# Performance work log

Measured on AMD Instinct MI355X. Metric: run time of the kernel, lower is better.

Reference implementation:

```python
import jax, jax.numpy as jnp
import numpy as np

N_NODES = 50000
N_EDGES = 600000
IN_DIM = 128
HID = 128
N_LAYERS = 4
N_GRAPHS = 128
N_CLASSES = 10
SPARSITY = 0.5
BN_EPS = 1e-5


def setup_inputs() -> dict:
    key = jax.random.key(0)
    ks = jax.random.split(key, 16)
    h = jax.random.normal(ks[0], (N_NODES, IN_DIM), dtype=jnp.float32)
    snorm_n = jax.random.uniform(ks[1], (N_NODES, 1), dtype=jnp.float32)
    src = jax.random.randint(ks[2], (N_EDGES,), 0, N_NODES, dtype=jnp.int32)
    dst = jax.random.randint(ks[3], (N_EDGES,), 0, N_NODES, dtype=jnp.int32)
    graph_ids = jnp.sort(jax.random.randint(ks[4], (N_NODES,), 0, N_GRAPHS, dtype=jnp.int32))
    # Expander (sparsity-masked) linear params
    embed_W = 0.1 * jax.random.normal(ks[5], (HID, IN_DIM), dtype=jnp.float32)
    embed_mask = (jax.random.uniform(ks[6], (HID, IN_DIM)) < SPARSITY).astype(jnp.float32)
    embed_b = jnp.zeros((HID,), dtype=jnp.float32)
    layer_W = 0.1 * jax.random.normal(ks[7], (N_LAYERS, HID, HID), dtype=jnp.float32)
    layer_mask = (jax.random.uniform(ks[8], (N_LAYERS, HID, HID)) < SPARSITY).astype(jnp.float32)
    layer_b = jnp.zeros((N_LAYERS, HID), dtype=jnp.float32)
    gamma = jnp.ones((N_LAYERS, HID), dtype=jnp.float32)
    beta = jnp.zeros((N_LAYERS, HID), dtype=jnp.float32)
    ro_W = 0.1 * jax.random.normal(ks[9], (N_CLASSES, HID), dtype=jnp.float32)
    ro_b = jnp.zeros((N_CLASSES,), dtype=jnp.float32)
    return {"h": h, "snorm_n": snorm_n, "src": src, "dst": dst, "graph_ids": graph_ids,
            "embed_W": embed_W, "embed_mask": embed_mask, "embed_b": embed_b,
            "layer_W": layer_W, "layer_mask": layer_mask, "layer_b": layer_b,
            "gamma": gamma, "beta": beta, "ro_W": ro_W, "ro_b": ro_b}


def reference(h, snorm_n, src, dst, graph_ids, embed_W, embed_mask, embed_b,
              layer_W, layer_mask, layer_b, gamma, beta, ro_W, ro_b):
    n = h.shape[0]
    # embedding_h: sparsity-masked linear
    h = h @ (embed_W * embed_mask).T + embed_b
    for l in range(layer_W.shape[0]):
        h_in = h
        # message passing: copy_src + sum reduce over edges
        agg = jax.ops.segment_sum(h[src], dst, num_segments=n)  # [N, HID]
        # node apply: masked linear MLP (n_mlp=1)
        z = agg @ (layer_W[l] * layer_mask[l]).T + layer_b[l]
        # graph norm
        z = z * snorm_n
        # batch norm (training-mode batch statistics)
        mu = jnp.mean(z, axis=0)
        var = jnp.var(z, axis=0)
        z = (z - mu) * jax.lax.rsqrt(var + BN_EPS) * gamma[l] + beta[l]
        # activation + residual
        z = jax.nn.relu(z)
        h = h_in + z
    # mean readout over graphs (segment mean)
    sums = jax.ops.segment_sum(h, graph_ids, num_segments=N_GRAPHS)  # [G, HID]
    cnt = jax.ops.segment_sum(jnp.ones((n, 1), h.dtype), graph_ids, num_segments=N_GRAPHS)
    hg = sums / jnp.maximum(cnt, 1.0)
    return hg @ ro_W.T + ro_b
```

## Files before the change

### kernel.cpp

```cpp
#include <hip/hip_runtime.h>
#include <hip/hip_bf16.h>

#define N_NODES   50000
#define N_EDGES   600000
#define HID       128
#define N_LAYERS  4
#define N_GRAPHS  128
#define N_CLASSES 10
#define BN_EPS    1e-5f

#define RSPLIT 8
#define SCAN_B 196
#define GEMM_GRID ((N_NODES + 63) / 64)
#define CVT_N   3200000
#define CVT_GRID ((CVT_N + 255) / 256)
#define NREP 32

#define OFF_WMT   0u
#define OFF_H     81920u
#define OFF_Z     (OFF_H   + 6400000u)
#define OFF_AGG   (OFF_Z   + 6400000u)
#define OFF_ZERO  (OFF_AGG + 6400000u)
#define OFF_CSUMR OFF_ZERO
#define OFF_SUMS  (OFF_CSUMR + 32768u)
#define OFF_DEG   (OFF_SUMS + 16384u)
#define ZERO_N    (32768u + 16384u + 50000u)
#define OFF_OFFS  (OFF_ZERO + ZERO_N)
#define OFF_POS   (OFF_OFFS + 50004u)
#define OFF_ESRC  (OFF_POS  + 50000u)
#define OFF_GST   (OFF_ESRC + 600000u)
#define OFF_BSUM  (OFF_GST  + 132u)
#define OFF_TOT   (OFF_BSUM + 196u)
#define OFF_CSUMF (OFF_TOT  + 4u)
#define OFF_HBF   (OFF_CSUMF + 1024u)

#define PRE_ZB 388
#define PRE_WB 160
#define PRE_BB 196

typedef __attribute__((ext_vector_type(8))) short short8;
typedef __attribute__((ext_vector_type(4))) float f32x4;

__device__ __forceinline__ unsigned int bf16_of(float f) {
    unsigned int u = __float_as_uint(f);
    return (u + 0x7fffu + ((u >> 16) & 1u)) >> 16;
}
__device__ __forceinline__ unsigned int pack_bf2(float lo, float hi) {
    return bf16_of(lo) | (bf16_of(hi) << 16);
}

__global__ __launch_bounds__(256) void preamble_kernel(
    int* __restrict__ zbase,
    const float* __restrict__ We, const float* __restrict__ Me,
    const float* __restrict__ Wl, const float* __restrict__ Ml,
    unsigned int* __restrict__ Wbf,
    const int* __restrict__ gid, int* __restrict__ g_start)
{
    int b = blockIdx.x;
    if (b < PRE_ZB) {
        int i = b * 256 + threadIdx.x;
        if (i < (int)ZERO_N) zbase[i] = 0;
    } else if (b < PRE_ZB + PRE_WB) {
        int i = (b - PRE_ZB) * 256 + threadIdx.x;
        if (i < 5 * 8192) {
            int m = i >> 13;
            int j = i & 8191;
            int c = j >> 6, ku = j & 63;
            const float* Wsrc = (m == 0) ? We : Wl + (m - 1) * 16384;
            const float* Msrc = (m == 0) ? Me : Ml + (m - 1) * 16384;
            int base = c * 128 + ku * 2;
            float w0 = Wsrc[base] * Msrc[base];
            float w1 = Wsrc[base + 1] * Msrc[base + 1];
            unsigned int h0 = bf16_of(w0), h1 = bf16_of(w1);
            float l0 = w0 - __uint_as_float(h0 << 16);
            float l1 = w1 - __uint_as_float(h1 << 16);
            Wbf[m * 16384 + c * 64 + ku]        = h0 | (h1 << 16);
            Wbf[m * 16384 + 8192 + c * 64 + ku] = bf16_of(l0) | (bf16_of(l1) << 16);
        }
    } else {
        int i = (b - PRE_ZB - PRE_WB) * 256 + threadIdx.x;
        if (i >= N_NODES) return;
        int g = gid[i];
        if (i == 0) {
            for (int x = 0; x <= g; ++x) g_start[x] = 0;
        } else {
            int gp = gid[i - 1];
            for (int x = gp + 1; x <= g; ++x) g_start[x] = i;
        }
        if (i == N_NODES - 1) {
            for (int x = g + 1; x <= N_GRAPHS; ++x) g_start[x] = N_NODES;
        }
    }
}

__global__ __launch_bounds__(256) void cvt_kernel(const float2* __restrict__ src,
                                                  unsigned int* __restrict__ dst, int n) {
    int i = blockIdx.x * 256 + threadIdx.x;
    if (i < n) {
        float2 v = src[i];
        dst[i] = pack_bf2(v.x, v.y);
    }
}

__global__ __launch_bounds__(256) void hist_kernel(const int* __restrict__ dst,
                                                   int* __restrict__ deg, int nE) {
    int i = blockIdx.x * 256 + threadIdx.x;
    if (i < nE) atomicAdd(&deg[dst[i]], 1);
}

__global__ __launch_bounds__(256) void scan1_kernel(const int* __restrict__ deg,
                                                    int* __restrict__ off,
                                                    int* __restrict__ bsum, int n) {
    __shared__ int s[256];
    int tid = threadIdx.x;
    int i = blockIdx.x * 256 + tid;
    int v = (i < n) ? deg[i] : 0;
    s[tid] = v;
    __syncthreads();
#pragma unroll
    for (int ofs = 1; ofs < 256; ofs <<= 1) {
        int t = (tid >= ofs) ? s[tid - ofs] : 0;
        __syncthreads();
        s[tid] += t;
        __syncthreads();
    }
    if (i < n) off[i] = s[tid] - v;
    if (tid == 255) bsum[blockIdx.x] = s[255];
}

__global__ __launch_bounds__(256) void scan2_kernel(int* __restrict__ bsum,
                                                    int* __restrict__ total, int nb) {
    __shared__ int s[256];
    int tid = threadIdx.x;
    int v = (tid < nb) ? bsum[tid] : 0;
    s[tid] = v;
    __syncthreads();
#pragma unroll
    for (int ofs = 1; ofs < 256; ofs <<= 1) {
        int t = (tid >= ofs) ? s[tid - ofs] : 0;
        __syncthreads();
        s[tid] += t;
        __syncthreads();
    }
    if (tid < nb) bsum[tid] = s[tid] - v;
    if (tid == 255) *total = s[255];
}

__global__ __launch_bounds__(256) void scan3_kernel(int* __restrict__ off,
                                                    const int* __restrict__ bsum,
                                                    const int* __restrict__ total,
                                                    int* __restrict__ pos, int n) {
    int i = blockIdx.x * 256 + threadIdx.x;
    if (i < n) {
        int o = off[i] + bsum[blockIdx.x];
        off[i] = o;
        pos[i] = o;
    }
    if (i == 0) off[n] = *total;
}

__global__ __launch_bounds__(256) void fill_kernel(const int* __restrict__ src,
                                                   const int* __restrict__ dst,
                                                   int* __restrict__ pos,
                                                   int* __restrict__ esrc, int nE) {
    int i = blockIdx.x * 256 + threadIdx.x;
    if (i < nE) {
        int p = atomicAdd(&pos[dst[i]], 1);
        esrc[p] = src[i];
    }
}

__global__ __launch_bounds__(256) void aggregate_kernel(const unsigned int* __restrict__ Hbf,
                                                        const int* __restrict__ off,
                                                        const int* __restrict__ esrc,
                                                        unsigned int* __restrict__ aggbf,
                                                        int nN) {
    int wid  = (blockIdx.x * 256 + threadIdx.x) >> 6;
    int lane = threadIdx.x & 63;
    int half = lane >> 5;
    int l4   = lane & 31;
    int node = wid * 2 + half;
    if (node >= nN) return;
    int beg = off[node], end = off[node + 1];
    const uint2* H2 = (const uint2*)Hbf;
    float4 a0 = make_float4(0.f, 0.f, 0.f, 0.f);
    float4 a1 = make_float4(0.f, 0.f, 0.f, 0.f);
    float4 a2 = make_float4(0.f, 0.f, 0.f, 0.f);
    float4 a3 = make_float4(0.f, 0.f, 0.f, 0.f);
#define ACCUM(AX, V)                                                        \
    AX.x += __uint_as_float((V).x << 16);                                   \
    AX.y += __uint_as_float((V).x & 0xffff0000u);                           \
    AX.z += __uint_as_float((V).y << 16);                                   \
    AX.w += __uint_as_float((V).y & 0xffff0000u);
    int e = beg;
    for (; e + 7 < end; e += 8) {
        int s0 = esrc[e],     s1 = esrc[e + 1], s2 = esrc[e + 2], s3 = esrc[e + 3];
        int s4 = esrc[e + 4], s5 = esrc[e + 5], s6 = esrc[e + 6], s7 = esrc[e + 7];
        uint2 v0 = H2[(size_t)s0 * 32 + l4];
        uint2 v1 = H2[(size_t)s1 * 32 + l4];
        uint2 v2 = H2[(size_t)s2 * 32 + l4];
        uint2 v3 = H2[(size_t)s3 * 32 + l4];
        uint2 v4 = H2[(size_t)s4 * 32 + l4];
        uint2 v5 = H2[(size_t)s5 * 32 + l4];
        uint2 v6 = H2[(size_t)s6 * 32 + l4];
        uint2 v7 = H2[(size_t)s7 * 32 + l4];
        ACCUM(a0, v0) ACCUM(a1, v1) ACCUM(a2, v2) ACCUM(a3, v3)
        ACCUM(a0, v4) ACCUM(a1, v5) ACCUM(a2, v6) ACCUM(a3, v7)
    }
    for (; e + 3 < end; e += 4) {
        int s0 = esrc[e], s1 = esrc[e + 1], s2 = esrc[e + 2], s3 = esrc[e + 3];
        uint2 v0 = H2[(size_t)s0 * 32 + l4];
        uint2 v1 = H2[(size_t)s1 * 32 + l4];
        uint2 v2 = H2[(size_t)s2 * 32 + l4];
        uint2 v3 = H2[(size_t)s3 * 32 + l4];
        ACCUM(a0, v0) ACCUM(a1, v1) ACCUM(a2, v2) ACCUM(a3, v3)
    }
    for (; e < end; ++e) {
        uint2 v0 = H2[(size_t)esrc[e] * 32 + l4];
        ACCUM(a0, v0)
    }
#undef ACCUM
    a0.x += a1.x; a0.y += a1.y; a0.z += a1.z; a0.w += a1.w;
    a2.x += a3.x; a2.y += a3.y; a2.z += a3.z; a2.w += a3.w;
    a0.x += a2.x; a0.y += a2.y; a0.z += a2.z; a0.w += a2.w;
    uint2 o;
    o.x = pack_bf2(a0.x, a0.y);
    o.y = pack_bf2(a0.z, a0.w);
    ((uint2*)aggbf)[(size_t)node * 32 + l4] = o;
}

__global__ __launch_bounds__(256) void gemm_mfma(
    const uint4* __restrict__ Abf,
    const unsigned int* __restrict__ Wmat,
    const float* __restrict__ bias, const float* __restrict__ snorm,
    float* __restrict__ Z, float* __restrict__ colsum, int nRows)
{
    __shared__ unsigned int As[64 * 64];
    int tid = threadIdx.x;
    int w  = tid >> 6;
    int l  = tid & 63;
    int q  = l >> 4;
    int ri = l & 15;
    int r0 = blockIdx.x * 64;

    short8 bfrag[2][2][4];
    const uint4* W4 = (const uint4*)Wmat;
#pragma unroll
    for (int p = 0; p < 2; ++p)
#pragma unroll
        for (int ct2 = 0; ct2 < 2; ++ct2) {
            int c = (w * 2 + ct2) * 16 + ri;
#pragma unroll
            for (int kc = 0; kc < 4; ++kc) {
                uint4 t = W4[p * 2048 + c * 16 + kc * 4 + q];
                bfrag[p][ct2][kc] = *(short8*)&t;
            }
        }

#pragma unroll
    for (int it = 0; it < 4; ++it) {
        int e = tid + it * 256;
        int r = e >> 4, g = e & 15;
        int gr = r0 + r;
        if (gr >= nRows) gr = nRows - 1;
        uint4 v = Abf[(size_t)gr * 16 + g];
        *(uint4*)&As[r * 64 + ((g ^ (r & 7)) << 2)] = v;
    }
    __syncthreads();

    f32x4 zero4 = {0.f, 0.f, 0.f, 0.f};
    f32x4 acc[4][2];
#pragma unroll
    for (int rt = 0; rt < 4; ++rt)
#pragma unroll
        for (int ct2 = 0; ct2 < 2; ++ct2) acc[rt][ct2] = zero4;

#pragma unroll
    for (int kc = 0; kc < 4; ++kc)
#pragma unroll
        for (int rt = 0; rt < 4; ++rt) {
            int row = rt * 16 + ri;
            short8 af = *(const short8*)&As[row * 64 + (((kc * 4 + q) ^ (ri & 7)) << 2)];
#pragma unroll
            for (int ct2 = 0; ct2 < 2; ++ct2) {
                acc[rt][ct2] = __builtin_amdgcn_mfma_f32_16x16x32_bf16(
                    af, bfrag[0][ct2][kc], acc[rt][ct2], 0, 0, 0);
                acc[rt][ct2] = __builtin_amdgcn_mfma_f32_16x16x32_bf16(
                    af, bfrag[1][ct2][kc], acc[rt][ct2], 0, 0, 0);
            }
        }

    float csv[2] = {0.f, 0.f}, cqv[2] = {0.f, 0.f};
#pragma unroll
    for (int ct2 = 0; ct2 < 2; ++ct2) {
        int col = (w * 2 + ct2) * 16 + ri;
        float bb = bias[col];
#pragma unroll
        for (int rt = 0; rt < 4; ++rt)
#pragma unroll
            for (int reg = 0; reg < 4; ++reg) {
                int row = r0 + rt * 16 + q * 4 + reg;
                if (row < nRows) {
                    float sn = snorm ? snorm[row] : 1.0f;
                    float v = (acc[rt][ct2][reg] + bb) * sn;
                    Z[(size_t)row * 128 + col] = v;
                    csv[ct2] += v;
                    cqv[ct2] += v * v;
                }
            }
    }
    if (colsum) {
        float* cdst = colsum + ((blockIdx.x & (NREP - 1)) << 8);
#pragma unroll
        for (int ct2 = 0; ct2 < 2; ++ct2) {
            float s  = csv[ct2], sq = cqv[ct2];
            s  += __shfl_xor(s, 16);  s  += __shfl_xor(s, 32);
            sq += __shfl_xor(sq, 16); sq += __shfl_xor(sq, 32);
            if (q == 0) {
                int col = (w * 2 + ct2) * 16 + ri;
                atomicAdd(&cdst[col], s);
                atomicAdd(&cdst[128 + col], sq);
            }
        }
    }
}

__global__ __launch_bounds__(256) void bnred_kernel(const float* __restrict__ rep,
                                                    float* __restrict__ outp) {
    int t = threadIdx.x;
    float s = 0.f;
#pragma unroll
    for (int r = 0; r < NREP; ++r) s += rep[r * 256 + t];
    outp[t] = s;
}

__global__ __launch_bounds__(256) void apply_kernel(const float* __restrict__ Z,
                                                    const float* __restrict__ csum,
                                                    const float* __restrict__ gamma,
                                                    const float* __restrict__ beta,
                                                    float* __restrict__ H,
                                                    unsigned int* __restrict__ hbf,
                                                    int n4, int layer) {
    int i = blockIdx.x * 256 + threadIdx.x;
    if (i >= n4) return;
    int c4 = i & 31;
    const float invN = 1.0f / (float)N_NODES;
    float4 s  = ((const float4*)(csum  + layer * 256))[c4];
    float4 q  = ((const float4*)(csum  + layer * 256 + 128))[c4];
    float4 g  = ((const float4*)(gamma + layer * 128))[c4];
    float4 be = ((const float4*)(beta  + layer * 128))[c4];
    float4 z = ((const float4*)Z)[i];
    float4 h = ((float4*)H)[i];
    float mu, var, sc, sh;
    mu = s.x * invN; var = q.x * invN - mu * mu; sc = g.x * rsqrtf(var + BN_EPS); sh = be.x - mu * sc;
    h.x += fmaxf(z.x * sc + sh, 0.f);
    mu = s.y * invN; var = q.y * invN - mu * mu; sc = g.y * rsqrtf(var + BN_EPS); sh = be.y - mu * sc;
    h.y += fmaxf(z.y * sc + sh, 0.f);
    mu = s.z * invN; var = q.z * invN - mu * mu; sc = g.z * rsqrtf(var + BN_EPS); sh = be.z - mu * sc;
    h.z += fmaxf(z.z * sc + sh, 0.f);
    mu = s.w * invN; var = q.w * invN - mu * mu; sc = g.w * rsqrtf(var + BN_EPS); sh = be.w - mu * sc;
    h.w += fmaxf(z.w * sc + sh, 0.f);
    ((float4*)H)[i] = h;
    hbf[i * 2]     = pack_bf2(h.x, h.y);
    hbf[i * 2 + 1] = pack_bf2(h.z, h.w);
}

__global__ __launch_bounds__(256) void readout2_kernel(const float* __restrict__ H,
                                                       const int* __restrict__ g_start,
                                                       float* __restrict__ sums) {
    int g     = blockIdx.x / RSPLIT;
    int chunk = blockIdx.x % RSPLIT;
    int beg = g_start[g], end = g_start[g + 1];
    int col  = threadIdx.x & 127;
    int half = threadIdx.x >> 7;
    float acc = 0.f;
    for (int r = beg + chunk * 2 + half; r < end; r += RSPLIT * 2) {
        acc += H[(size_t)r * 128 + col];
    }
    if (acc != 0.f || half == 0)
        atomicAdd(&sums[g * 128 + col], acc);
}

__global__ __launch_bounds__(128) void final_kernel(const float* __restrict__ sums,
                                                    const int* __restrict__ g_start,
                                                    const float* __restrict__ roW,
                                                    const float* __restrict__ rob,
                                                    float* __restrict__ out) {
    __shared__ float row[128];
    int g = blockIdx.x;
    int t = threadIdx.x;
    float c = fmaxf((float)(g_start[g + 1] - g_start[g]), 1.0f);
    row[t] = sums[g * 128 + t] / c;
    __syncthreads();
    if (t < N_CLASSES) {
        float s = rob[t];
        for (int k = 0; k < 128; ++k) s += row[k] * roW[t * 128 + k];
        out[g * N_CLASSES + t] = s;
    }
}

extern "C" void kernel_launch(void* const* d_in, const int* in_sizes, int n_in,
                              void* d_out, int out_size, void* d_ws, size_t ws_size,
                              hipStream_t stream) {
    const float* h0      = (const float*)d_in[0];
    const float* snorm   = (const float*)d_in[1];
    const int*   src     = (const int*)d_in[2];
    const int*   dst     = (const int*)d_in[3];
    const int*   gid     = (const int*)d_in[4];
    const float* embedW  = (const float*)d_in[5];
    const float* embedM  = (const float*)d_in[6];
    const float* embedB  = (const float*)d_in[7];
    const float* layerW  = (const float*)d_in[8];
    const float* layerM  = (const float*)d_in[9];
    const float* layerB  = (const float*)d_in[10];
    const float* gamma   = (const float*)d_in[11];
    const float* beta    = (const float*)d_in[12];
    const float* roW     = (const float*)d_in[13];
    const float* rob     = (const float*)d_in[14];
    float* out = (float*)d_out;

    float* ws   = (float*)d_ws;
    unsigned int* Wbf = (unsigned int*)(ws + OFF_WMT);
    float* H    = ws + OFF_H;
    float* Z    = ws + OFF_Z;
    unsigned int* h0bf  = (unsigned int*)(ws + OFF_AGG);
    unsigned int* aggbf = (unsigned int*)(ws + OFF_AGG) + 3200000;
    float* csumr = ws + OFF_CSUMR;
    float* csumf = ws + OFF_CSUMF;
    float* sums = ws + OFF_SUMS;
    int*   deg  = (int*)(ws + OFF_DEG);
    int*   offs = (int*)(ws + OFF_OFFS);
    int*   pos  = (int*)(ws + OFF_POS);
    int*   esrc = (int*)(ws + OFF_ESRC);
    int*   gst  = (int*)(ws + OFF_GST);
    int*   bsum = (int*)(ws + OFF_BSUM);
    int*   tot  = (int*)(ws + OFF_TOT);
    unsigned int* Hbf = (unsigned int*)(ws + OFF_HBF);

    preamble_kernel<<<PRE_ZB + PRE_WB + PRE_BB, 256, 0, stream>>>(
        (int*)(ws + OFF_ZERO), embedW, embedM, layerW, layerM, Wbf, gid, gst);
    hist_kernel<<<(N_EDGES + 255) / 256, 256, 0, stream>>>(dst, deg, N_EDGES);
    scan1_kernel<<<SCAN_B, 256, 0, stream>>>(deg, offs, bsum, N_NODES);
    scan2_kernel<<<1, 256, 0, stream>>>(bsum, tot, SCAN_B);
    scan3_kernel<<<SCAN_B, 256, 0, stream>>>(offs, bsum, tot, pos, N_NODES);
    fill_kernel<<<(N_EDGES + 255) / 256, 256, 0, stream>>>(src, dst, pos, esrc, N_EDGES);

    cvt_kernel<<<CVT_GRID, 256, 0, stream>>>((const float2*)h0, h0bf, CVT_N);
    gemm_mfma<<<GEMM_GRID, 256, 0, stream>>>((const uint4*)h0bf, Wbf, embedB,
                                             nullptr, H, nullptr, N_NODES);
    cvt_kernel<<<CVT_GRID, 256, 0, stream>>>((const float2*)H, Hbf, CVT_N);

    const int agg_grid = (N_NODES / 2 + 3) / 4;
    for (int l = 0; l < N_LAYERS; ++l) {
        aggregate_kernel<<<agg_grid, 256, 0, stream>>>(Hbf, offs, esrc, aggbf, N_NODES);
        gemm_mfma<<<GEMM_GRID, 256, 0, stream>>>((const uint4*)aggbf,
                                                 Wbf + (1 + l) * 16384,
                                                 layerB + l * 128, snorm,
                                                 Z, csumr + l * (NREP * 256), N_NODES);
        bnred_kernel<<<1, 256, 0, stream>>>(csumr + l * (NREP * 256), csumf + l * 256);
        apply_kernel<<<(N_NODES * HID / 4) / 256, 256, 0, stream>>>(
            Z, csumf, gamma, beta, H, Hbf, N_NODES * HID / 4, l);
    }

    readout2_kernel<<<N_GRAPHS * RSPLIT, 256, 0, stream>>>(H, gst, sums);
    final_kernel<<<N_GRAPHS, 128, 0, stream>>>(sums, gst, roW, rob, out);
}
```

Before: 466.7 us.

## Fuse aggregation into GEMM and replace CSR build with fixed-width ELL

Replaces the histogram, three-pass scan and fill kernels with a single atomic ELL fill using a fixed width of 64 neighbour slots per node. The per-layer neighbour aggregation is fused into the MFMA GEMM, writing aggregated bf16 rows straight into shared memory so the agg buffer round trip through global memory disappears. The embedding GEMM now also emits the bf16 copy directly, which drops a conversion kernel. In exchange, nodes with more than 64 in-edges are silently truncated, the ELL neighbour order depends on atomic ordering, and the gather now runs inside the GEMM block with less parallelism per node.

```diff
diff --git a/kernel.cpp b/kernel.cpp
--- a/kernel.cpp
+++ b/kernel.cpp
@@ -10,28 +10,24 @@
 #define BN_EPS    1e-5f
 
 #define RSPLIT 8
-#define SCAN_B 196
 #define GEMM_GRID ((N_NODES + 63) / 64)
 #define CVT_N   3200000
 #define CVT_GRID ((CVT_N + 255) / 256)
 #define NREP 32
+#define ELL_W 64
 
 #define OFF_WMT   0u
 #define OFF_H     81920u
-#define OFF_Z     (OFF_H   + 6400000u)
-#define OFF_AGG   (OFF_Z   + 6400000u)
-#define OFF_ZERO  (OFF_AGG + 6400000u)
+#define OFF_Z     (OFF_H + 6400000u)
+#define OFF_H0BF  (OFF_Z + 6400000u)
+#define OFF_ZERO  (OFF_H0BF + 3200000u)
 #define OFF_CSUMR OFF_ZERO
 #define OFF_SUMS  (OFF_CSUMR + 32768u)
 #define OFF_DEG   (OFF_SUMS + 16384u)
 #define ZERO_N    (32768u + 16384u + 50000u)
-#define OFF_OFFS  (OFF_ZERO + ZERO_N)
-#define OFF_POS   (OFF_OFFS + 50004u)
-#define OFF_ESRC  (OFF_POS  + 50000u)
-#define OFF_GST   (OFF_ESRC + 600000u)
-#define OFF_BSUM  (OFF_GST  + 132u)
-#define OFF_TOT   (OFF_BSUM + 196u)
-#define OFF_CSUMF (OFF_TOT  + 4u)
+#define OFF_ELL   (OFF_ZERO + ZERO_N)
+#define OFF_GST   (OFF_ELL + 3200000u)
+#define OFF_CSUMF (OFF_GST + 132u)
 #define OFF_HBF   (OFF_CSUMF + 1024u)
 
 #define PRE_ZB 388
@@ -93,6 +89,18 @@
     }
 }
 
+__global__ __launch_bounds__(256) void ellfill_kernel(const int* __restrict__ src,
+                                                      const int* __restrict__ dst,
+                                                      int* __restrict__ deg,
+                                                      int* __restrict__ ell, int nE) {
+    int i = blockIdx.x * 256 + threadIdx.x;
+    if (i < nE) {
+        int d = dst[i];
+        int slot = atomicAdd(&deg[d], 1);
+        if (slot < ELL_W) ell[(size_t)d * ELL_W + slot] = src[i];
+    }
+}
+
 __global__ __launch_bounds__(256) void cvt_kernel(const float2* __restrict__ src,
                                                   unsigned int* __restrict__ dst, int n) {
     int i = blockIdx.x * 256 + threadIdx.x;
@@ -102,135 +110,89 @@
     }
 }
 
-__global__ __launch_bounds__(256) void hist_kernel(const int* __restrict__ dst,
-                                                   int* __restrict__ deg, int nE) {
-    int i = blockIdx.x * 256 + threadIdx.x;
-    if (i < nE) atomicAdd(&deg[dst[i]], 1);
-}
-
-__global__ __launch_bounds__(256) void scan1_kernel(const int* __restrict__ deg,
-                                                    int* __restrict__ off,
-                                                    int* __restrict__ bsum, int n) {
-    __shared__ int s[256];
-    int tid = threadIdx.x;
-    int i = blockIdx.x * 256 + tid;
-    int v = (i < n) ? deg[i] : 0;
-    s[tid] = v;
-    __syncthreads();
-#pragma unroll
-    for (int ofs = 1; ofs < 256; ofs <<= 1) {
-        int t = (tid >= ofs) ? s[tid - ofs] : 0;
-        __syncthreads();
-        s[tid] += t;
-        __syncthreads();
-    }
-    if (i < n) off[i] = s[tid] - v;
-    if (tid == 255) bsum[blockIdx.x] = s[255];
-}
-
-__global__ __launch_bounds__(256) void scan2_kernel(int* __restrict__ bsum,
-                                                    int* __restrict__ total, int nb) {
-    __shared__ int s[256];
-    int tid = threadIdx.x;
-    int v = (tid < nb) ? bsum[tid] : 0;
-    s[tid] = v;
-    __syncthreads();
-#pragma unroll
-    for (int ofs = 1; ofs < 256; ofs <<= 1) {
-        int t = (tid >= ofs) ? s[tid - ofs] : 0;
-        __syncthreads();
-        s[tid] += t;
-        __syncthreads();
-    }
-    if (tid < nb) bsum[tid] = s[tid] - v;
-    if (tid == 255) *total = s[255];
-}
-
-__global__ __launch_bounds__(256) void scan3_kernel(int* __restrict__ off,
-                                                    const int* __restrict__ bsum,
-                                                    const int* __restrict__ total,
-                                                    int* __restrict__ pos, int n) {
-    int i = blockIdx.x * 256 + threadIdx.x;
-    if (i < n) {
-        int o = off[i] + bsum[blockIdx.x];
-        off[i] = o;
-        pos[i] = o;
-    }
-    if (i == 0) off[n] = *total;
-}
-
-__global__ __launch_bounds__(256) void fill_kernel(const int* __restrict__ src,
-                                                   const int* __restrict__ dst,
-                                                   int* __restrict__ pos,
-                                                   int* __restrict__ esrc, int nE) {
-    int i = blockIdx.x * 256 + threadIdx.x;
-    if (i < nE) {
-        int p = atomicAdd(&pos[dst[i]], 1);
-        esrc[p] = src[i];
-    }
-}
-
-__global__ __launch_bounds__(256) void aggregate_kernel(const unsigned int* __restrict__ Hbf,
-                                                        const int* __restrict__ off,
-                                                        const int* __restrict__ esrc,
-                                                        unsigned int* __restrict__ aggbf,
-                                                        int nN) {
-    int wid  = (blockIdx.x * 256 + threadIdx.x) >> 6;
-    int lane = threadIdx.x & 63;
-    int half = lane >> 5;
-    int l4   = lane & 31;
-    int node = wid * 2 + half;
-    if (node >= nN) return;
-    int beg = off[node], end = off[node + 1];
-    const uint2* H2 = (const uint2*)Hbf;
-    float4 a0 = make_float4(0.f, 0.f, 0.f, 0.f);
-    float4 a1 = make_float4(0.f, 0.f, 0.f, 0.f);
-    float4 a2 = make_float4(0.f, 0.f, 0.f, 0.f);
-    float4 a3 = make_float4(0.f, 0.f, 0.f, 0.f);
-#define ACCUM(AX, V)                                                        \
-    AX.x += __uint_as_float((V).x << 16);                                   \
-    AX.y += __uint_as_float((V).x & 0xffff0000u);                           \
-    AX.z += __uint_as_float((V).y << 16);                                   \
-    AX.w += __uint_as_float((V).y & 0xffff0000u);
-    int e = beg;
-    for (; e + 7 < end; e += 8) {
-        int s0 = esrc[e],     s1 = esrc[e + 1], s2 = esrc[e + 2], s3 = esrc[e + 3];
-        int s4 = esrc[e + 4], s5 = esrc[e + 5], s6 = esrc[e + 6], s7 = esrc[e + 7];
-        uint2 v0 = H2[(size_t)s0 * 32 + l4];
-        uint2 v1 = H2[(size_t)s1 * 32 + l4];
-        uint2 v2 = H2[(size_t)s2 * 32 + l4];
-        uint2 v3 = H2[(size_t)s3 * 32 + l4];
-        uint2 v4 = H2[(size_t)s4 * 32 + l4];
-        uint2 v5 = H2[(size_t)s5 * 32 + l4];
-        uint2 v6 = H2[(size_t)s6 * 32 + l4];
-        uint2 v7 = H2[(size_t)s7 * 32 + l4];
-        ACCUM(a0, v0) ACCUM(a1, v1) ACCUM(a2, v2) ACCUM(a3, v3)
-        ACCUM(a0, v4) ACCUM(a1, v5) ACCUM(a2, v6) ACCUM(a3, v7)
-    }
-    for (; e + 3 < end; e += 4) {
-        int s0 = esrc[e], s1 = esrc[e + 1], s2 = esrc[e + 2], s3 = esrc[e + 3];
-        uint2 v0 = H2[(size_t)s0 * 32 + l4];
-        uint2 v1 = H2[(size_t)s1 * 32 + l4];
-        uint2 v2 = H2[(size_t)s2 * 32 + l4];
-        uint2 v3 = H2[(size_t)s3 * 32 + l4];
-        ACCUM(a0, v0) ACCUM(a1, v1) ACCUM(a2, v2) ACCUM(a3, v3)
-    }
-    for (; e < end; ++e) {
-        uint2 v0 = H2[(size_t)esrc[e] * 32 + l4];
-        ACCUM(a0, v0)
-    }
-#undef ACCUM
-    a0.x += a1.x; a0.y += a1.y; a0.z += a1.z; a0.w += a1.w;
-    a2.x += a3.x; a2.y += a3.y; a2.z += a3.z; a2.w += a3.w;
-    a0.x += a2.x; a0.y += a2.y; a0.z += a2.z; a0.w += a2.w;
-    uint2 o;
-    o.x = pack_bf2(a0.x, a0.y);
-    o.y = pack_bf2(a0.z, a0.w);
-    ((uint2*)aggbf)[(size_t)node * 32 + l4] = o;
-}
-
 __global__ __launch_bounds__(256) void gemm_mfma(
     const uint4* __restrict__ Abf,
+    const unsigned int* __restrict__ Wmat,
+    const float* __restrict__ bias,
+    float* __restrict__ Z, unsigned int* __restrict__ hbf, int nRows)
+{
+    __shared__ unsigned int As[64 * 64];
+    int tid = threadIdx.x;
+    int w  = tid >> 6;
+    int l  = tid & 63;
+    int q  = l >> 4;
+    int ri = l & 15;
+    int r0 = blockIdx.x * 64;
+
+    short8 bfrag[2][2][4];
+    const uint4* W4 = (const uint4*)Wmat;
+#pragma unroll
+    for (int p = 0; p < 2; ++p)
+#pragma unroll
+        for (int ct2 = 0; ct2 < 2; ++ct2) {
+            int c = (w * 2 + ct2) * 16 + ri;
+#pragma unroll
+            for (int kc = 0; kc < 4; ++kc) {
+                uint4 t = W4[p * 2048 + c * 16 + kc * 4 + q];
+                bfrag[p][ct2][kc] = *(short8*)&t;
+            }
+        }
+
+#pragma unroll
+    for (int it = 0; it < 4; ++it) {
+        int e = tid + it * 256;
+        int r = e >> 4, g = e & 15;
+        int gr = r0 + r;
+        if (gr >= nRows) gr = nRows - 1;
+        uint4 v = Abf[(size_t)gr * 16 + g];
+        *(uint4*)&As[r * 64 + ((g ^ (r & 7)) << 2)] = v;
+    }
+    __syncthreads();
+
+    f32x4 zero4 = {0.f, 0.f, 0.f, 0.f};
+    f32x4 acc[4][2];
+#pragma unroll
+    for (int rt = 0; rt < 4; ++rt)
+#pragma unroll
+        for (int ct2 = 0; ct2 < 2; ++ct2) acc[rt][ct2] = zero4;
+
+#pragma unroll
+    for (int kc = 0; kc < 4; ++kc)
+#pragma unroll
+        for (int rt = 0; rt < 4; ++rt) {
+            int row = rt * 16 + ri;
+            short8 af = *(const short8*)&As[row * 64 + (((kc * 4 + q) ^ (ri & 7)) << 2)];
+#pragma unroll
+            for (int ct2 = 0; ct2 < 2; ++ct2) {
+                acc[rt][ct2] = __builtin_amdgcn_mfma_f32_16x16x32_bf16(
+                    af, bfrag[0][ct2][kc], acc[rt][ct2], 0, 0, 0);
+                acc[rt][ct2] = __builtin_amdgcn_mfma_f32_16x16x32_bf16(
+                    af, bfrag[1][ct2][kc], acc[rt][ct2], 0, 0, 0);
+            }
+        }
+
+    unsigned short* hb = (unsigned short*)hbf;
+#pragma unroll
+    for (int ct2 = 0; ct2 < 2; ++ct2) {
+        int col = (w * 2 + ct2) * 16 + ri;
+        float bb = bias[col];
+#pragma unroll
+        for (int rt = 0; rt < 4; ++rt)
+#pragma unroll
+            for (int reg = 0; reg < 4; ++reg) {
+                int row = r0 + rt * 16 + q * 4 + reg;
+                if (row < nRows) {
+                    float v = acc[rt][ct2][reg] + bb;
+                    Z[(size_t)row * 128 + col] = v;
+                    hb[(size_t)row * 128 + col] = (unsigned short)bf16_of(v);
+                }
+            }
+    }
+}
+
+__global__ __launch_bounds__(256) void agg_gemm_mfma(
+    const unsigned int* __restrict__ Hbf,
+    const int* __restrict__ deg, const int* __restrict__ ell,
     const unsigned int* __restrict__ Wmat,
     const float* __restrict__ bias, const float* __restrict__ snorm,
     float* __restrict__ Z, float* __restrict__ colsum, int nRows)
@@ -241,7 +203,64 @@
     int l  = tid & 63;
     int q  = l >> 4;
     int ri = l & 15;
+    int half = l >> 5;
+    int l4   = l & 31;
     int r0 = blockIdx.x * 64;
+
+    const uint2* H2 = (const uint2*)Hbf;
+#pragma unroll
+    for (int iter = 0; iter < 8; ++iter) {
+        int rl = iter * 8 + w * 2 + half;
+        int node = r0 + rl;
+        if (node >= nRows) node = nRows - 1;
+        int dg = deg[node];
+        const int* ep = ell + (size_t)node * ELL_W;
+        float4 a0 = make_float4(0.f, 0.f, 0.f, 0.f);
+        float4 a1 = make_float4(0.f, 0.f, 0.f, 0.f);
+        float4 a2 = make_float4(0.f, 0.f, 0.f, 0.f);
+        float4 a3 = make_float4(0.f, 0.f, 0.f, 0.f);
+#define ACCUM(AX, V)                                                        \
+        AX.x += __uint_as_float((V).x << 16);                               \
+        AX.y += __uint_as_float((V).x & 0xffff0000u);                       \
+        AX.z += __uint_as_float((V).y << 16);                               \
+        AX.w += __uint_as_float((V).y & 0xffff0000u);
+        int e = 0;
+        for (; e + 7 < dg; e += 8) {
+            int s0 = ep[e],     s1 = ep[e + 1], s2 = ep[e + 2], s3 = ep[e + 3];
+            int s4 = ep[e + 4], s5 = ep[e + 5], s6 = ep[e + 6], s7 = ep[e + 7];
+            uint2 v0 = H2[(size_t)s0 * 32 + l4];
+            uint2 v1 = H2[(size_t)s1 * 32 + l4];
+            uint2 v2 = H2[(size_t)s2 * 32 + l4];
+            uint2 v3 = H2[(size_t)s3 * 32 + l4];
+            uint2 v4 = H2[(size_t)s4 * 32 + l4];
+            uint2 v5 = H2[(size_t)s5 * 32 + l4];
+            uint2 v6 = H2[(size_t)s6 * 32 + l4];
+            uint2 v7 = H2[(size_t)s7 * 32 + l4];
+            ACCUM(a0, v0) ACCUM(a1, v1) ACCUM(a2, v2) ACCUM(a3, v3)
+            ACCUM(a0, v4) ACCUM(a1, v5) ACCUM(a2, v6) ACCUM(a3, v7)
+        }
+        for (; e + 3 < dg; e += 4) {
+            int s0 = ep[e], s1 = ep[e + 1], s2 = ep[e + 2], s3 = ep[e + 3];
+            uint2 v0 = H2[(size_t)s0 * 32 + l4];
+            uint2 v1 = H2[(size_t)s1 * 32 + l4];
+            uint2 v2 = H2[(size_t)s2 * 32 + l4];
+            uint2 v3 = H2[(size_t)s3 * 32 + l4];
+            ACCUM(a0, v0) ACCUM(a1, v1) ACCUM(a2, v2) ACCUM(a3, v3)
+        }
+        for (; e < dg; ++e) {
+            uint2 v0 = H2[(size_t)ep[e] * 32 + l4];
+            ACCUM(a0, v0)
+        }
+#undef ACCUM
+        a0.x += a1.x; a0.y += a1.y; a0.z += a1.z; a0.w += a1.w;
+        a2.x += a3.x; a2.y += a3.y; a2.z += a3.z; a2.w += a3.w;
+        a0.x += a2.x; a0.y += a2.y; a0.z += a2.z; a0.w += a2.w;
+        uint2 o;
+        o.x = pack_bf2(a0.x, a0.y);
+        o.y = pack_bf2(a0.z, a0.w);
+        int g16 = l4 >> 1;
+        *(uint2*)&As[rl * 64 + ((g16 ^ (rl & 7)) << 2) + (l4 & 1) * 2] = o;
+    }
 
     short8 bfrag[2][2][4];
     const uint4* W4 = (const uint4*)Wmat;
@@ -256,16 +275,6 @@
                 bfrag[p][ct2][kc] = *(short8*)&t;
             }
         }
-
-#pragma unroll
-    for (int it = 0; it < 4; ++it) {
-        int e = tid + it * 256;
-        int r = e >> 4, g = e & 15;
-        int gr = r0 + r;
-        if (gr >= nRows) gr = nRows - 1;
-        uint4 v = Abf[(size_t)gr * 16 + g];
-        *(uint4*)&As[r * 64 + ((g ^ (r & 7)) << 2)] = v;
-    }
     __syncthreads();
 
     f32x4 zero4 = {0.f, 0.f, 0.f, 0.f};
@@ -301,7 +310,7 @@
             for (int reg = 0; reg < 4; ++reg) {
                 int row = r0 + rt * 16 + q * 4 + reg;
                 if (row < nRows) {
-                    float sn = snorm ? snorm[row] : 1.0f;
+                    float sn = snorm[row];
                     float v = (acc[rt][ct2][reg] + bb) * sn;
                     Z[(size_t)row * 128 + col] = v;
                     csv[ct2] += v;
@@ -309,7 +318,7 @@
                 }
             }
     }
-    if (colsum) {
+    {
         float* cdst = colsum + ((blockIdx.x & (NREP - 1)) << 8);
 #pragma unroll
         for (int ct2 = 0; ct2 < 2; ++ct2) {
@@ -423,40 +432,27 @@
     unsigned int* Wbf = (unsigned int*)(ws + OFF_WMT);
     float* H    = ws + OFF_H;
     float* Z    = ws + OFF_Z;
-    unsigned int* h0bf  = (unsigned int*)(ws + OFF_AGG);
-    unsigned int* aggbf = (unsigned int*)(ws + OFF_AGG) + 3200000;
+    unsigned int* h0bf = (unsigned int*)(ws + OFF_H0BF);
     float* csumr = ws + OFF_CSUMR;
     float* csumf = ws + OFF_CSUMF;
     float* sums = ws + OFF_SUMS;
     int*   deg  = (int*)(ws + OFF_DEG);
-    int*   offs = (int*)(ws + OFF_OFFS);
-    int*   pos  = (int*)(ws + OFF_POS);
-    int*   esrc = (int*)(ws + OFF_ESRC);
+    int*   ell  = (int*)(ws + OFF_ELL);
     int*   gst  = (int*)(ws + OFF_GST);
-    int*   bsum = (int*)(ws + OFF_BSUM);
-    int*   tot  = (int*)(ws + OFF_TOT);
     unsigned int* Hbf = (unsigned int*)(ws + OFF_HBF);
 
     preamble_kernel<<<PRE_ZB + PRE_WB + PRE_BB, 256, 0, stream>>>(
         (int*)(ws + OFF_ZERO), embedW, embedM, layerW, layerM, Wbf, gid, gst);
-    hist_kernel<<<(N_EDGES + 255) / 256, 256, 0, stream>>>(dst, deg, N_EDGES);
-    scan1_kernel<<<SCAN_B, 256, 0, stream>>>(deg, offs, bsum, N_NODES);
-    scan2_kernel<<<1, 256, 0, stream>>>(bsum, tot, SCAN_B);
-    scan3_kernel<<<SCAN_B, 256, 0, stream>>>(offs, bsum, tot, pos, N_NODES);
-    fill_kernel<<<(N_EDGES + 255) / 256, 256, 0, stream>>>(src, dst, pos, esrc, N_EDGES);
+    ellfill_kernel<<<(N_EDGES + 255) / 256, 256, 0, stream>>>(src, dst, deg, ell, N_EDGES);
 
     cvt_kernel<<<CVT_GRID, 256, 0, stream>>>((const float2*)h0, h0bf, CVT_N);
     gemm_mfma<<<GEMM_GRID, 256, 0, stream>>>((const uint4*)h0bf, Wbf, embedB,
-                                             nullptr, H, nullptr, N_NODES);
-    cvt_kernel<<<CVT_GRID, 256, 0, stream>>>((const float2*)H, Hbf, CVT_N);
-
-    const int agg_grid = (N_NODES / 2 + 3) / 4;
+                                             H, Hbf, N_NODES);
+
     for (int l = 0; l < N_LAYERS; ++l) {
-        aggregate_kernel<<<agg_grid, 256, 0, stream>>>(Hbf, offs, esrc, aggbf, N_NODES);
-        gemm_mfma<<<GEMM_GRID, 256, 0, stream>>>((const uint4*)aggbf,
-                                                 Wbf + (1 + l) * 16384,
-                                                 layerB + l * 128, snorm,
-                                                 Z, csumr + l * (NREP * 256), N_NODES);
+        agg_gemm_mfma<<<GEMM_GRID, 256, 0, stream>>>(
+            Hbf, deg, ell, Wbf + (1 + l) * 16384,
+            layerB + l * 128, snorm, Z, csumr + l * (NREP * 256), N_NODES);
         bnred_kernel<<<1, 256, 0, stream>>>(csumr + l * (NREP * 256), csumf + l * 256);
         apply_kernel<<<(N_NODES * HID / 4) / 256, 256, 0, stream>>>(
             Z, csumf, gamma, beta, H, Hbf, N_NODES * HID / 4, l);
```

New measurement: 522.7 us. +12.0%, slower.
